# Performance work log

Hardware: AMD Instinct MI355X
Metric: run time of the kernel (lower is better)

Reference implementation:

```python
import jax, jax.numpy as jnp
import numpy as np
import math

B, S, D, H = 4, 1024, 1024, 16
DK = D // H


def setup_inputs() -> dict:
    key = jax.random.key(0)
    ks = jax.random.split(key, 12)
    inp = {
        "q": jax.random.normal(ks[0], (B, S, D), jnp.float32),
        "k": jax.random.normal(ks[1], (B, S, D), jnp.float32),
        "v": jax.random.normal(ks[2], (B, S, D), jnp.float32),
        # causal mask, broadcast over batch (0 = masked)
        "mask": jnp.broadcast_to(jnp.tril(jnp.ones((S, S), jnp.int32)), (B, S, S)),
    }
    sc = 1.0 / math.sqrt(D)
    # torch nn.Linear convention: y = x @ W.T + b, W:[out,in]
    inp["Wq"] = jax.random.normal(ks[3], (D, D), jnp.float32) * sc
    inp["bq"] = jnp.zeros((D,), jnp.float32)
    inp["Wk"] = jax.random.normal(ks[4], (D, D), jnp.float32) * sc
    inp["bk"] = jnp.zeros((D,), jnp.float32)
    inp["Wv"] = jax.random.normal(ks[5], (D, D), jnp.float32) * sc
    inp["bv"] = jnp.zeros((D,), jnp.float32)
    inp["Wo"] = jax.random.normal(ks[6], (D, D), jnp.float32) * sc
    inp["bo"] = jnp.zeros((D,), jnp.float32)
    return inp


def _mha(q, k, v, mask, Wq, bq, Wk, bk, Wv, bv, Wo, bo):
    def split_heads(x):  # [B,S,D] -> [B,H,S,DK]
        return x.reshape(B, S, H, DK).transpose(0, 2, 1, 3)

    qh = split_heads(q @ Wq.T + bq)
    kh = split_heads(k @ Wk.T + bk)
    vh = split_heads(v @ Wv.T + bv)

    scores = jnp.einsum("bhqd,bhkd->bhqk", qh, kh) / math.sqrt(DK)
    scores = jnp.where(mask[:, None, :, :] == 0, jnp.float32(-1e9), scores)
    weights = jax.nn.softmax(scores, axis=-1)  # dropout in eval mode -> identity
    out = jnp.einsum("bhqk,bhkd->bhqd", weights, vh)
    out = out.transpose(0, 2, 1, 3).reshape(B, S, D)
    return out @ Wo.T + bo


def reference(q, k, v, mask, Wq, bq, Wk, bk, Wv, bv, Wo, bo):
    return _mha(q, k, v, mask, Wq, bq, Wk, bk, Wv, bv, Wo, bo)
```

## Files before the change

kernel.cpp:

```cpp
#include <hip/hip_runtime.h>

typedef unsigned short u16;
typedef __bf16 bf16x8 __attribute__((ext_vector_type(8)));
typedef float floatx4 __attribute__((ext_vector_type(4)));

#define BB 4
#define SS 1024
#define DD 1024
#define HH 16
#define DKK 64
#define MM (BB*SS)

__device__ __forceinline__ u16 f2bf(float f) {
    union { float f; unsigned int u; } v; v.f = f;
    unsigned int r = v.u + 0x7fffu + ((v.u >> 16) & 1u);
    return (u16)(r >> 16);
}

__device__ __forceinline__ void async16(const u16* g, u16* l) {
    __builtin_amdgcn_global_load_lds(
        (const __attribute__((address_space(1))) void*)g,
        (__attribute__((address_space(3))) void*)l,
        16, 0, 0);
}

__global__ __launch_bounds__(256) void convert_kernel(
    const float* __restrict__ q, const float* __restrict__ k, const float* __restrict__ v,
    const float* __restrict__ Wq, const float* __restrict__ Wk, const float* __restrict__ Wv,
    const float* __restrict__ Wo,
    u16* qb, u16* kb, u16* vb, u16* Wqb, u16* Wkb, u16* Wvb, u16* Wob) {
    const int Q4 = (BB*SS*DD) / 4;
    const int W4 = (DD*DD) / 4;
    int idx = blockIdx.x * 256 + threadIdx.x;
    const float* src; u16* dst; int off;
    if (idx < Q4)            { src = q; dst = qb; off = idx; }
    else if (idx < 2*Q4)     { src = k; dst = kb; off = idx - Q4; }
    else if (idx < 3*Q4)     { src = v; dst = vb; off = idx - 2*Q4; }
    else {
        int r = idx - 3*Q4;
        int wsel = r / W4; off = r - wsel*W4;
        src = wsel==0 ? Wq : wsel==1 ? Wk : wsel==2 ? Wv : Wo;
        dst = wsel==0 ? Wqb : wsel==1 ? Wkb : wsel==2 ? Wvb : Wob;
    }
    float4 x = ((const float4*)src)[off];
    ushort4 y;
    y.x = f2bf(x.x); y.y = f2bf(x.y); y.z = f2bf(x.z); y.w = f2bf(x.w);
    ((ushort4*)dst)[off] = y;
}

__global__ __launch_bounds__(256) void qkv_gemm(
    const u16* __restrict__ qb, const u16* __restrict__ kb, const u16* __restrict__ vb,
    const u16* __restrict__ Wqb, const u16* __restrict__ Wkb, const u16* __restrict__ Wvb,
    const float* __restrict__ bq, const float* __restrict__ bk, const float* __restrict__ bv,
    u16* Qh, u16* Kh, u16* Vt) {
    const int K = DD;
    __shared__ u16 sA[128*32];
    __shared__ u16 sW[128*32];
    int nb = blockIdx.x;
    int m0 = blockIdx.y * 128;
    int which = nb >> 3;
    int n0 = (nb & 7) * 128;
    const u16* A   = which==0 ? qb  : which==1 ? kb  : vb;
    const u16* W   = which==0 ? Wqb : which==1 ? Wkb : Wvb;
    const float* bias = which==0 ? bq : which==1 ? bk : bv;
    u16* Out = which==0 ? Qh : which==1 ? Kh : Vt;
    float scale = which==0 ? 0.125f : 1.0f;

    int t = threadIdx.x;
    int w = t >> 6, l = t & 63, g = l >> 4, c = l & 15;
    int wm = w & 1, wn = w >> 1;
    int sw = (g ^ (c & 3)) * 8;

    floatx4 acc[4][4] = {};

    int srow = t >> 2;
    int sseg = (t & 3) ^ (srow & 3);
    const u16* gA0 = A + (size_t)(m0 + srow) * K + sseg*8;
    const u16* gW0 = W + (size_t)(n0 + srow) * K + sseg*8;
    u16* lA = &sA[t*8];
    u16* lW = &sW[t*8];

    for (int kk = 0; kk < K; kk += 32) {
        __syncthreads();
        async16(gA0 + kk,          lA);
        async16(gA0 + 64*K + kk,   lA + 64*32);
        async16(gW0 + kk,          lW);
        async16(gW0 + 64*K + kk,   lW + 64*32);
        __syncthreads();
        bf16x8 af[4], bf_[4];
        #pragma unroll
        for (int i = 0; i < 4; i++) af[i]  = *(const bf16x8*)&sA[(wm*64 + i*16 + c)*32 + sw];
        #pragma unroll
        for (int j = 0; j < 4; j++) bf_[j] = *(const bf16x8*)&sW[(wn*64 + j*16 + c)*32 + sw];
        #pragma unroll
        for (int i = 0; i < 4; i++)
            #pragma unroll
            for (int j = 0; j < 4; j++)
                acc[i][j] = __builtin_amdgcn_mfma_f32_16x16x32_bf16(af[i], bf_[j], acc[i][j], 0, 0, 0);
    }

    #pragma unroll
    for (int j = 0; j < 4; j++) {
        int col = n0 + wn*64 + j*16 + c;
        float bb = bias[col];
        int h = col >> 6, dk = col & 63;
        #pragma unroll
        for (int i = 0; i < 4; i++) {
            #pragma unroll
            for (int r = 0; r < 4; r++) {
                int row = m0 + wm*64 + i*16 + g*4 + r;
                int b = row >> 10, s = row & 1023;
                float vv = (acc[i][j][r] + bb) * scale;
                u16 bits = f2bf(vv);
                if (which == 2) {
                    Out[((size_t)((b*HH + h)*DKK + dk))*SS + s] = bits;
                } else {
                    Out[((size_t)(b*HH + h)*SS + s)*DKK + dk] = bits;
                }
            }
        }
    }
}

__global__ __launch_bounds__(256) void attn_kernel(
    const u16* __restrict__ Qh, const u16* __restrict__ Kh, const u16* __restrict__ Vt,
    u16* __restrict__ attnO) {
    __shared__ u16 sQ[64*64];
    __shared__ u16 sK[2][64*64];
    __shared__ u16 sVt[2][64*64];
    __shared__ u16 sP[64*72];

    int bh = blockIdx.y;
    const u16* Qp  = Qh + (size_t)bh * SS * DKK;
    const u16* Kp  = Kh + (size_t)bh * SS * DKK;
    const u16* Vtp = Vt + (size_t)bh * DKK * SS;
    int b = bh >> 4, h = bh & 15;

    int t = threadIdx.x, w = t >> 6, l = t & 63, g = l >> 4, c = l & 15;
    int wq = w * 16;
    int cx = c & 7;

    int qi0 = t, qi1 = t + 256;
    int r0 = qi0 >> 3, s0 = (qi0 & 7) ^ (r0 & 7);
    int r1 = qi1 >> 3, s1 = (qi1 & 7) ^ (r1 & 7);

    #pragma unroll
    for (int phase = 0; phase < 2; phase++) {
        int qt = phase == 0 ? (15 - (int)blockIdx.x) : (int)blockIdx.x;
        int q0 = qt * 64;

        __syncthreads();
        async16(&Qp[(q0 + r0)*DKK + s0*8], &sQ[qi0*8]);
        async16(&Qp[(q0 + r1)*DKK + s1*8], &sQ[qi1*8]);
        async16(&Kp[(r0)*DKK + s0*8],      &sK[0][qi0*8]);
        async16(&Kp[(r1)*DKK + s1*8],      &sK[0][qi1*8]);
        async16(&Vtp[r0*SS + s0*8],        &sVt[0][qi0*8]);
        async16(&Vtp[r1*SS + s1*8],        &sVt[0][qi1*8]);

        float l_[4] = {0.f, 0.f, 0.f, 0.f};
        floatx4 o[4] = {};
        int cur = 0;

        for (int k0 = 0; k0 <= q0; k0 += 64) {
            __syncthreads();
            int kn = k0 + 64;
            if (kn <= q0) {
                async16(&Kp[(kn + r0)*DKK + s0*8], &sK[cur^1][qi0*8]);
                async16(&Kp[(kn + r1)*DKK + s1*8], &sK[cur^1][qi1*8]);
                async16(&Vtp[r0*SS + kn + s0*8],   &sVt[cur^1][qi0*8]);
                async16(&Vtp[r1*SS + kn + s1*8],   &sVt[cur^1][qi1*8]);
            }

            floatx4 sc_[4] = {};
            #pragma unroll
            for (int ks = 0; ks < 2; ks++) {
                int so = ((ks*4 + g) ^ cx) * 8;
                bf16x8 aq = *(const bf16x8*)&sQ[(wq + c)*64 + so];
                #pragma unroll
                for (int nt = 0; nt < 4; nt++) {
                    bf16x8 bk_ = *(const bf16x8*)&sK[cur][(nt*16 + c)*64 + so];
                    sc_[nt] = __builtin_amdgcn_mfma_f32_16x16x32_bf16(aq, bk_, sc_[nt], 0, 0, 0);
                }
            }

            if (k0 == q0) {
                #pragma unroll
                for (int nt = 0; nt < 4; nt++)
                    #pragma unroll
                    for (int r = 0; r < 4; r++) {
                        int qg = wq + g*4 + r;
                        int kg = nt*16 + c;
                        if (kg > qg) sc_[nt][r] = -1e30f;
                    }
            }

            #pragma unroll
            for (int r = 0; r < 4; r++) {
                float rs = 0.f;
                #pragma unroll
                for (int nt = 0; nt < 4; nt++) {
                    float p = __expf(sc_[nt][r]);
                    sc_[nt][r] = p;
                    rs += p;
                }
                rs += __shfl_xor(rs, 1);
                rs += __shfl_xor(rs, 2);
                rs += __shfl_xor(rs, 4);
                rs += __shfl_xor(rs, 8);
                l_[r] += rs;
                int prow = (wq + g*4 + r)*72;
                #pragma unroll
                for (int nt = 0; nt < 4; nt++)
                    sP[prow + nt*16 + c] = f2bf(sc_[nt][r]);
            }

            #pragma unroll
            for (int ks = 0; ks < 2; ks++) {
                int so = ((ks*4 + g) ^ cx) * 8;
                bf16x8 ap = *(const bf16x8*)&sP[(wq + c)*72 + ks*32 + g*8];
                #pragma unroll
                for (int nt = 0; nt < 4; nt++) {
                    bf16x8 bv_ = *(const bf16x8*)&sVt[cur][(nt*16 + c)*64 + so];
                    o[nt] = __builtin_amdgcn_mfma_f32_16x16x32_bf16(ap, bv_, o[nt], 0, 0, 0);
                }
            }
            cur ^= 1;
        }

        #pragma unroll
        for (int r = 0; r < 4; r++) {
            float inv = 1.0f / l_[r];
            int row = q0 + wq + g*4 + r;
            #pragma unroll
            for (int nt = 0; nt < 4; nt++) {
                int dcol = h*64 + nt*16 + c;
                attnO[((size_t)b*SS + row)*DD + dcol] = f2bf(o[nt][r] * inv);
            }
        }
    }
}

__global__ __launch_bounds__(256) void out_gemm(
    const u16* __restrict__ A, const u16* __restrict__ W,
    const float* __restrict__ bo, float* __restrict__ out) {
    const int K = DD;
    __shared__ u16 sA[64*32];
    __shared__ u16 sW[128*32];
    int n0 = blockIdx.x * 128;
    int m0 = blockIdx.y * 64;

    int t = threadIdx.x;
    int w = t >> 6, l = t & 63, g = l >> 4, c = l & 15;
    int wm = w & 1, wn = w >> 1;
    int sw = (g ^ (c & 3)) * 8;

    floatx4 acc[2][4] = {};

    int srow = t >> 2;
    int sseg = (t & 3) ^ (srow & 3);
    const u16* gA0 = A + (size_t)(m0 + srow) * K + sseg*8;
    const u16* gW0 = W + (size_t)(n0 + srow) * K + sseg*8;
    u16* lA = &sA[t*8];
    u16* lW = &sW[t*8];

    for (int kk = 0; kk < K; kk += 32) {
        __syncthreads();
        async16(gA0 + kk,        lA);
        async16(gW0 + kk,        lW);
        async16(gW0 + 64*K + kk, lW + 64*32);
        __syncthreads();
        bf16x8 af[2], bf_[4];
        #pragma unroll
        for (int i = 0; i < 2; i++) af[i]  = *(const bf16x8*)&sA[(wm*32 + i*16 + c)*32 + sw];
        #pragma unroll
        for (int j = 0; j < 4; j++) bf_[j] = *(const bf16x8*)&sW[(wn*64 + j*16 + c)*32 + sw];
        #pragma unroll
        for (int i = 0; i < 2; i++)
            #pragma unroll
            for (int j = 0; j < 4; j++)
                acc[i][j] = __builtin_amdgcn_mfma_f32_16x16x32_bf16(af[i], bf_[j], acc[i][j], 0, 0, 0);
    }

    #pragma unroll
    for (int j = 0; j < 4; j++) {
        int col = n0 + wn*64 + j*16 + c;
        float bb = bo[col];
        #pragma unroll
        for (int i = 0; i < 2; i++) {
            #pragma unroll
            for (int r = 0; r < 4; r++) {
                int row = m0 + wm*32 + i*16 + g*4 + r;
                out[(size_t)row*DD + col] = acc[i][j][r] + bb;
            }
        }
    }
}

extern "C" void kernel_launch(void* const* d_in, const int* in_sizes, int n_in,
                              void* d_out, int out_size, void* d_ws, size_t ws_size,
                              hipStream_t stream) {
    const float* q    = (const float*)d_in[0];
    const float* k    = (const float*)d_in[1];
    const float* v    = (const float*)d_in[2];
    const float* Wq   = (const float*)d_in[4];
    const float* bq   = (const float*)d_in[5];
    const float* Wk   = (const float*)d_in[6];
    const float* bk   = (const float*)d_in[7];
    const float* Wv   = (const float*)d_in[8];
    const float* bv   = (const float*)d_in[9];
    const float* Wo   = (const float*)d_in[10];
    const float* bo   = (const float*)d_in[11];
    float* out = (float*)d_out;

    char* ws = (char*)d_ws;
    const size_t MB = 1024*1024;
    u16* qb   = (u16*)(ws + 0*MB);
    u16* kb   = (u16*)(ws + 8*MB);
    u16* vb   = (u16*)(ws + 16*MB);
    u16* Wqb  = (u16*)(ws + 24*MB);
    u16* Wkb  = (u16*)(ws + 26*MB);
    u16* Wvb  = (u16*)(ws + 28*MB);
    u16* Wob  = (u16*)(ws + 30*MB);
    u16* Qh   = (u16*)(ws + 32*MB);
    u16* Kh   = (u16*)(ws + 40*MB);
    u16* Vt   = (u16*)(ws + 48*MB);
    u16* attn = (u16*)(ws + 56*MB);

    convert_kernel<<<16384, 256, 0, stream>>>(q, k, v, Wq, Wk, Wv, Wo,
                                              qb, kb, vb, Wqb, Wkb, Wvb, Wob);
    qkv_gemm<<<dim3(24, 32), 256, 0, stream>>>(qb, kb, vb, Wqb, Wkb, Wvb,
                                               bq, bk, bv, Qh, Kh, Vt);
    attn_kernel<<<dim3(8, 64), 256, 0, stream>>>(Qh, Kh, Vt, attn);
    out_gemm<<<dim3(8, 64), 256, 0, stream>>>(attn, Wob, bo, out);
}
```

Baseline: 225.2 us.

## Compute softmax row sums via MFMA with ones vector and remap QKV grid

The attention kernel no longer sums probabilities with per-row shuffle reductions. It adds one extra MFMA per k-step that multiplies the bf16 P tile by a ones column and reads the row sum from lane 0 of each group at the end. The sum now uses the bf16-rounded probabilities, which matches what the P·V product sees but slightly changes the numerics. Separately, the QKV GEMM block index is remapped so consecutive blocks group M tiles together for better L2 reuse of the weight and activation tiles.

```diff
diff --git a/kernel.cpp b/kernel.cpp
--- a/kernel.cpp
+++ b/kernel.cpp
@@ -56,10 +56,17 @@
     const int K = DD;
     __shared__ u16 sA[128*32];
     __shared__ u16 sW[128*32];
-    int nb = blockIdx.x;
-    int m0 = blockIdx.y * 128;
-    int which = nb >> 3;
-    int n0 = (nb & 7) * 128;
+
+    int flat = blockIdx.x + 24 * blockIdx.y;
+    int qg  = flat >> 6;
+    int rem = flat & 63;
+    int nB  = rem >> 3;
+    int x8  = rem & 7;
+    int wmi = (qg << 3) | x8;
+    int which = wmi >> 5;
+    int m0 = (wmi & 31) * 128;
+    int n0 = nB * 128;
+
     const u16* A   = which==0 ? qb  : which==1 ? kb  : vb;
     const u16* W   = which==0 ? Wqb : which==1 ? Wkb : Wvb;
     const float* bias = which==0 ? bq : which==1 ? bk : bv;
@@ -140,6 +147,14 @@
     int wq = w * 16;
     int cx = c & 7;
 
+    bf16x8 bones;
+    {
+        __bf16 one = (__bf16)1.0f, zero = (__bf16)0.0f;
+        __bf16 val = (c == 0) ? one : zero;
+        #pragma unroll
+        for (int j = 0; j < 8; j++) bones[j] = val;
+    }
+
     int qi0 = t, qi1 = t + 256;
     int r0 = qi0 >> 3, s0 = (qi0 & 7) ^ (r0 & 7);
     int r1 = qi1 >> 3, s1 = (qi1 & 7) ^ (r1 & 7);
@@ -157,8 +172,8 @@
         async16(&Vtp[r0*SS + s0*8],        &sVt[0][qi0*8]);
         async16(&Vtp[r1*SS + s1*8],        &sVt[0][qi1*8]);
 
-        float l_[4] = {0.f, 0.f, 0.f, 0.f};
         floatx4 o[4] = {};
+        floatx4 ol = {};
         int cur = 0;
 
         for (int k0 = 0; k0 <= q0; k0 += 64) {
@@ -196,22 +211,12 @@
 
             #pragma unroll
             for (int r = 0; r < 4; r++) {
-                float rs = 0.f;
+                int prow = (wq + g*4 + r)*72;
                 #pragma unroll
                 for (int nt = 0; nt < 4; nt++) {
                     float p = __expf(sc_[nt][r]);
-                    sc_[nt][r] = p;
-                    rs += p;
+                    sP[prow + nt*16 + c] = f2bf(p);
                 }
-                rs += __shfl_xor(rs, 1);
-                rs += __shfl_xor(rs, 2);
-                rs += __shfl_xor(rs, 4);
-                rs += __shfl_xor(rs, 8);
-                l_[r] += rs;
-                int prow = (wq + g*4 + r)*72;
-                #pragma unroll
-                for (int nt = 0; nt < 4; nt++)
-                    sP[prow + nt*16 + c] = f2bf(sc_[nt][r]);
             }
 
             #pragma unroll
@@ -223,13 +228,15 @@
                     bf16x8 bv_ = *(const bf16x8*)&sVt[cur][(nt*16 + c)*64 + so];
                     o[nt] = __builtin_amdgcn_mfma_f32_16x16x32_bf16(ap, bv_, o[nt], 0, 0, 0);
                 }
+                ol = __builtin_amdgcn_mfma_f32_16x16x32_bf16(ap, bones, ol, 0, 0, 0);
             }
             cur ^= 1;
         }
 
         #pragma unroll
         for (int r = 0; r < 4; r++) {
-            float inv = 1.0f / l_[r];
+            float lv = __shfl(ol[r], l & 48);
+            float inv = 1.0f / lv;
             int row = q0 + wq + g*4 + r;
             #pragma unroll
             for (int nt = 0; nt < 4; nt++) {
```

After: 216.1 us. 4.0% less time.
